# Kernel optimization log

Hardware: AMD Instinct MI355X
Metric: run time of the kernel (lower is better)

Reference implementation:

```python
import math
import jax, jax.numpy as jnp
import numpy as np

B, T, C, H, E, K = 2, 2048, 1024, 16, 8, 2
HID = 4 * C
D = C // H

def new_gelu(x):
    return 0.5 * x * (1.0 + jnp.tanh(math.sqrt(2.0 / math.pi) * (x + 0.044715 * x ** 3)))

def layer_norm(x, g, b, eps=1e-5):
    mu = jnp.mean(x, axis=-1, keepdims=True)
    var = jnp.var(x, axis=-1, keepdims=True)
    return (x - mu) / jnp.sqrt(var + eps) * g + b

def setup_inputs():
    key = jax.random.key(0)
    ks = jax.random.split(key, 8)
    s = 0.02
    return {
        'x': jax.random.normal(ks[0], (B, T, C), jnp.float32),
        'ln1_g': jnp.ones((C,), jnp.float32), 'ln1_b': jnp.zeros((C,), jnp.float32),
        'ln2_g': jnp.ones((C,), jnp.float32), 'ln2_b': jnp.zeros((C,), jnp.float32),
        'attn_w': (jax.random.normal(ks[1], (C, 3 * C), jnp.float32) * s),
        'attn_b': jnp.zeros((3 * C,), jnp.float32),
        'proj_w': (jax.random.normal(ks[2], (C, C), jnp.float32) * s),
        'proj_b': jnp.zeros((C,), jnp.float32),
        'router_w': (jax.random.normal(ks[3], (C, E), jnp.float32) * s),
        'fc_w': (jax.random.normal(ks[4], (E, C, HID), jnp.float32) * s),
        'fc_b': jnp.zeros((E, HID), jnp.float32),
        'pj_w': (jax.random.normal(ks[5], (E, HID, C), jnp.float32) * s),
        'pj_b': jnp.zeros((E, C), jnp.float32),
    }

def reference(x, ln1_g, ln1_b, ln2_g, ln2_b, attn_w, attn_b, proj_w, proj_b, router_w, fc_w, fc_b, pj_w, pj_b):
    # --- causal self-attention with residual ---
    h = layer_norm(x, ln1_g, ln1_b)
    qkv = h @ attn_w + attn_b                              # [B,T,3C]
    q, k, v = jnp.split(qkv, 3, axis=-1)
    q = q.reshape(B, T, H, D).transpose(0, 2, 1, 3)        # [B,H,T,D]
    k = k.reshape(B, T, H, D).transpose(0, 2, 1, 3)
    v = v.reshape(B, T, H, D).transpose(0, 2, 1, 3)
    att = jnp.einsum('bhqd,bhkd->bhqk', q, k) * (1.0 / math.sqrt(D))
    mask = jnp.tril(jnp.ones((T, T), dtype=bool))
    att = jnp.where(mask, att, jnp.float32(-jnp.inf))
    att = jax.nn.softmax(att, axis=-1)                     # dropout p=0 (eval)
    y = jnp.einsum('bhqk,bhkd->bhqd', att, v)
    y = y.transpose(0, 2, 1, 3).reshape(B, T, C)
    x = x + (y @ proj_w + proj_b)
    # --- MoE FFN with residual ---
    h2 = layer_norm(x, ln2_g, ln2_b).reshape(B * T, C)     # [N,C]
    logits = h2 @ router_w                                 # [N,E]
    probs = jax.nn.softmax(logits, axis=-1)
    topk_p, topk_i = jax.lax.top_k(probs, K)               # [N,K]
    topk_p = topk_p / jnp.sum(topk_p, axis=-1, keepdims=True)
    # dense combine weights: zero outside selected experts (same math as scatter)
    gate = jnp.zeros((B * T, E), h2.dtype).at[jnp.arange(B * T)[:, None], topk_i].add(topk_p)
    out = jnp.zeros_like(h2)
    for e in range(E):  # fixed small expert loop
        he = new_gelu(h2 @ fc_w[e] + fc_b[e])              # [N,HID]
        out = out + gate[:, e:e + 1] * (he @ pj_w[e] + pj_b[e])
    return x + out.reshape(B, T, C)
```

## Files before the change

### kernel.cpp

```cpp
#include <hip/hip_runtime.h>
#include <math.h>


typedef __bf16 b16v8 __attribute__((ext_vector_type(8)));
typedef float f32x4 __attribute__((ext_vector_type(4)));

#define MFMA(a, b, c) __builtin_amdgcn_mfma_f32_16x16x32_bf16(a, b, c, 0, 0, 0)

#define GLOAD_LDS16(g, l)                                          \
  __builtin_amdgcn_global_load_lds(                                \
      (const __attribute__((address_space(1))) void*)(g),          \
      (__attribute__((address_space(3))) void*)(l), 16, 0, 0)

constexpr int Bc = 2, Tc = 2048, Cc = 1024, Hc = 16, Dc = 64;
constexpr int Nc = Bc * Tc;
constexpr int HIDc = 4096;
constexpr int Ec = 8;
constexpr int NPAIR = Nc * 2;
constexpr int NRBMAX = NPAIR / 128 + Ec;
constexpr float LOG2E = 1.4426950408889634f;

__device__ inline unsigned short f32_bf16(float f) {
  union { float f; unsigned u; } x; x.f = f;
  unsigned r = x.u + 0x7fffu + ((x.u >> 16) & 1u);
  return (unsigned short)(r >> 16);
}

__device__ inline float gelu_f(float x) {
  float t = 2.3021188f * x * (1.f + 0.044715f * x * x);
  float e = __builtin_amdgcn_exp2f(-t);
  return x * __builtin_amdgcn_rcpf(1.f + e);
}

__device__ inline int swz32(int row, int g) {
  return row * 32 + ((g ^ ((row >> 1) & 3)) * 8);
}

__global__ __launch_bounds__(256) void convT_kernel(
    const float* __restrict__ src, unsigned short* __restrict__ dst,
    int K, int N) {
  const size_t sb = (size_t)blockIdx.z * K * N;
  const int n0 = blockIdx.x * 32, k0 = blockIdx.y * 32;
  __shared__ float t[32][33];
  const int tx = threadIdx.x & 31, ty = threadIdx.x >> 5;
#pragma unroll
  for (int j = 0; j < 4; ++j)
    t[ty + j * 8][tx] = src[sb + (size_t)(k0 + ty + j * 8) * N + n0 + tx];
  __syncthreads();
#pragma unroll
  for (int j = 0; j < 4; ++j)
    dst[sb + (size_t)(n0 + ty + j * 8) * K + k0 + tx] = f32_bf16(t[tx][ty + j * 8]);
}

__global__ __launch_bounds__(256) void ln1_kernel(
    const float* __restrict__ x, const float* __restrict__ g,
    const float* __restrict__ b, unsigned short* __restrict__ out) {
  const int row = blockIdx.x;
  const int tid = threadIdx.x;
  const float* xr = x + (size_t)row * Cc;
  float v[4]; float s = 0.f, q = 0.f;
#pragma unroll
  for (int j = 0; j < 4; ++j) { v[j] = xr[tid + j * 256]; s += v[j]; q += v[j] * v[j]; }
#pragma unroll
  for (int m = 1; m <= 32; m <<= 1) { s += __shfl_xor(s, m); q += __shfl_xor(q, m); }
  __shared__ float red[2][4];
  const int w = tid >> 6;
  if ((tid & 63) == 0) { red[0][w] = s; red[1][w] = q; }
  __syncthreads();
  s = red[0][0] + red[0][1] + red[0][2] + red[0][3];
  q = red[1][0] + red[1][1] + red[1][2] + red[1][3];
  const float mean = s * (1.f / Cc);
  const float var = q * (1.f / Cc) - mean * mean;
  const float rstd = rsqrtf(var + 1e-5f);
#pragma unroll
  for (int j = 0; j < 4; ++j) {
    int c = tid + j * 256;
    out[(size_t)row * Cc + c] = f32_bf16((v[j] - mean) * rstd * g[c] + b[c]);
  }
}

__global__ __launch_bounds__(256) void ln2_router_kernel(
    const float* __restrict__ x, const float* __restrict__ g,
    const float* __restrict__ b, const float* __restrict__ rw,
    unsigned short* __restrict__ out, int* __restrict__ tki, float* __restrict__ tkp) {
  const int row = blockIdx.x;
  const int tid = threadIdx.x;
  const float* xr = x + (size_t)row * Cc;
  float v[4]; float s = 0.f, q = 0.f;
#pragma unroll
  for (int j = 0; j < 4; ++j) { v[j] = xr[tid + j * 256]; s += v[j]; q += v[j] * v[j]; }
#pragma unroll
  for (int m = 1; m <= 32; m <<= 1) { s += __shfl_xor(s, m); q += __shfl_xor(q, m); }
  __shared__ float red[2][4];
  const int w = tid >> 6;
  if ((tid & 63) == 0) { red[0][w] = s; red[1][w] = q; }
  __syncthreads();
  s = red[0][0] + red[0][1] + red[0][2] + red[0][3];
  q = red[1][0] + red[1][1] + red[1][2] + red[1][3];
  const float mean = s * (1.f / Cc);
  const float var = q * (1.f / Cc) - mean * mean;
  const float rstd = rsqrtf(var + 1e-5f);
  float lg[8] = {0.f, 0.f, 0.f, 0.f, 0.f, 0.f, 0.f, 0.f};
#pragma unroll
  for (int j = 0; j < 4; ++j) {
    int c = tid + j * 256;
    float nv = (v[j] - mean) * rstd * g[c] + b[c];
    out[(size_t)row * Cc + c] = f32_bf16(nv);
    const float* rwc = rw + c * 8;
#pragma unroll
    for (int e = 0; e < 8; ++e) lg[e] += nv * rwc[e];
  }
#pragma unroll
  for (int m = 1; m <= 32; m <<= 1) {
#pragma unroll
    for (int e = 0; e < 8; ++e) lg[e] += __shfl_xor(lg[e], m);
  }
  __shared__ float rl[4][8];
  if ((tid & 63) == 0) {
#pragma unroll
    for (int e = 0; e < 8; ++e) rl[w][e] = lg[e];
  }
  __syncthreads();
  if (tid == 0) {
    float L[8];
#pragma unroll
    for (int e = 0; e < 8; ++e) L[e] = rl[0][e] + rl[1][e] + rl[2][e] + rl[3][e];
    int i1 = 0;
    for (int e = 1; e < 8; ++e) if (L[e] > L[i1]) i1 = e;
    int i2 = (i1 == 0) ? 1 : 0;
    for (int e = 0; e < 8; ++e) if (e != i1 && L[e] > L[i2]) i2 = e;
    float e2 = expf(L[i2] - L[i1]);
    float inv = 1.f / (1.f + e2);
    tki[row * 2] = i1; tki[row * 2 + 1] = i2;
    tkp[row * 2] = inv; tkp[row * 2 + 1] = e2 * inv;
  }
}

__global__ __launch_bounds__(256) void count_kernel(
    const int* __restrict__ tki, int* __restrict__ counts) {
  int n = blockIdx.x * 256 + threadIdx.x;
  if (n >= Nc) return;
  atomicAdd(&counts[tki[n * 2]], 1);
  atomicAdd(&counts[tki[n * 2 + 1]], 1);
}

__global__ void scan_kernel(const int* __restrict__ counts,
                            int* __restrict__ eoff, int* __restrict__ cursor,
                            int* __restrict__ tbl_e, int* __restrict__ tbl_r0,
                            int* __restrict__ tbl_n) {
  if (threadIdx.x == 0 && blockIdx.x == 0) {
    int s = 0, nb = 0;
    for (int e = 0; e < Ec; ++e) {
      eoff[e] = s; cursor[e] = s;
      for (int r = 0; r < counts[e]; r += 128) {
        tbl_e[nb] = e; tbl_r0[nb] = r; ++nb;
      }
      s += counts[e];
    }
    eoff[Ec] = s;
    *tbl_n = nb;
  }
}

__global__ __launch_bounds__(256) void assign_kernel(
    const int* __restrict__ tki, int* __restrict__ cursor,
    int* __restrict__ slot_tok, int* __restrict__ tok2slot) {
  int n = blockIdx.x * 256 + threadIdx.x;
  if (n >= Nc) return;
#pragma unroll
  for (int kk = 0; kk < 2; ++kk) {
    int e = tki[n * 2 + kk];
    int slot = atomicAdd(&cursor[e], 1);
    slot_tok[slot] = n;
    tok2slot[n * 2 + kk] = slot;
  }
}

struct GArgs {
  const unsigned short* A;
  const unsigned short* Bt;
  const float* bias;
  int M, N, K, lda, ldb, klen;
  size_t Bstride; int biasStride;
  const int* eoff;
  const int* slot_tok;
  const int* tbl_e;
  const int* tbl_r0;
  const int* tbl_n;
  float* outF;
  const float* resid;
  unsigned short* outB;
  unsigned short* outK;
  unsigned short* outV;
};

template <int MODE>
__global__ __launch_bounds__(256) void gemm128b(GArgs g) {
  int e = 0, s0 = 0, Meff = g.M, row0;
  if constexpr (MODE == 2 || MODE == 3) {
    if ((int)blockIdx.y >= *g.tbl_n) return;
    e = g.tbl_e[blockIdx.y];
    row0 = g.tbl_r0[blockIdx.y];
    s0 = g.eoff[e];
    Meff = g.eoff[e + 1] - s0;
  } else {
    row0 = blockIdx.y * 128;
  }
  const int kh = (MODE == 3) ? blockIdx.z : 0;
  const int col0 = blockIdx.x * 128;
  const int kbase = kh * g.klen;

  __shared__ __align__(16) unsigned short As[128 * 32];
  __shared__ __align__(16) unsigned short Bs[128 * 32];

  const int tid = threadIdx.x;
  const int lane = tid & 63, w = tid >> 6;
  const int wr = w >> 1, wc = w & 1;
  const int fr = lane & 15, fg = lane >> 4;

  const unsigned short* Bt = g.Bt + (size_t)e * g.Bstride;
  const float* bias = g.bias + (size_t)e * g.biasStride;

  size_t aaddr[2], baddr[2];
#pragma unroll
  for (int i = 0; i < 2; ++i) {
    int pos = i * 256 + tid;
    int r = pos >> 2;
    int c8 = ((pos & 3) ^ ((r >> 1) & 3)) * 8;
    int gr = row0 + r;
    if (gr >= Meff) gr = Meff - 1;
    int srcrow;
    if constexpr (MODE == 2) srcrow = g.slot_tok[s0 + gr];
    else if constexpr (MODE == 3) srcrow = s0 + gr;
    else srcrow = gr;
    aaddr[i] = (size_t)srcrow * g.lda + kbase + c8;
    baddr[i] = (size_t)(col0 + r) * g.ldb + kbase + c8;
  }

  auto STAGE = [&](int k0) {
#pragma unroll
    for (int i = 0; i < 2; ++i) {
      GLOAD_LDS16(g.A + aaddr[i] + k0, &As[i * 2048 + w * 512]);
      GLOAD_LDS16(Bt + baddr[i] + k0, &Bs[i * 2048 + w * 512]);
    }
  };

  f32x4 acc[4][4] = {};
  const int nt = g.klen / 32;

  for (int t = 0; t < nt; ++t) {
    if (t) __syncthreads();
    STAGE(t * 32);
    __syncthreads();
    b16v8 af[4], bf_[4];
#pragma unroll
    for (int mi = 0; mi < 4; ++mi)
      af[mi] = *(const b16v8*)&As[swz32(wr * 64 + mi * 16 + fr, fg)];
#pragma unroll
    for (int ni = 0; ni < 4; ++ni)
      bf_[ni] = *(const b16v8*)&Bs[swz32(wc * 64 + ni * 16 + fr, fg)];
#pragma unroll
    for (int mi = 0; mi < 4; ++mi)
#pragma unroll
      for (int ni = 0; ni < 4; ++ni)
        acc[mi][ni] = MFMA(af[mi], bf_[ni], acc[mi][ni]);
  }

  float* outF3 = nullptr;
  if constexpr (MODE == 3) outF3 = g.outF + (size_t)kh * NPAIR * Cc;

#pragma unroll
  for (int mi = 0; mi < 4; ++mi) {
#pragma unroll
    for (int ni = 0; ni < 4; ++ni) {
#pragma unroll
      for (int rr = 0; rr < 4; ++rr) {
        int row = row0 + wr * 64 + mi * 16 + fg * 4 + rr;
        int col = col0 + wc * 64 + ni * 16 + fr;
        if (row >= Meff) continue;
        float bval = bias[col];
        if constexpr (MODE == 3) { if (kh != 0) bval = 0.f; }
        float val = acc[mi][ni][rr] + bval;
        if constexpr (MODE == 0) {
          int bb = row >> 11, tt = row & (Tc - 1);
          int which = col >> 10, cj = col & (Cc - 1);
          int hd = cj >> 6, d = cj & 63;
          if (which == 0)
            g.outB[(((size_t)(bb * Hc + hd)) * Tc + tt) * Dc + d] = f32_bf16(val);
          else if (which == 1)
            g.outK[(((size_t)(bb * Hc + hd)) * Tc + tt) * Dc + d] = f32_bf16(val);
          else
            g.outV[(((size_t)(bb * Hc + hd)) * Dc + d) * Tc + tt] = f32_bf16(val);
        } else if constexpr (MODE == 1) {
          size_t o = (size_t)row * g.N + col;
          g.outF[o] = val + g.resid[o];
        } else if constexpr (MODE == 2) {
          g.outB[(size_t)(s0 + row) * g.N + col] = f32_bf16(gelu_f(val));
        } else {
          outF3[(size_t)(s0 + row) * g.N + col] = val;
        }
      }
    }
  }
}

__global__ __launch_bounds__(512) void attn_kernel(
    const unsigned short* __restrict__ q, const unsigned short* __restrict__ k,
    const unsigned short* __restrict__ v, unsigned short* __restrict__ y) {
  const int qt = blockIdx.x, bh = blockIdx.y;
  const int qbase = qt * 128;
  __shared__ __align__(16) unsigned short ldsK[64][72];
  __shared__ __align__(16) unsigned short ldsVT[64][72];
  __shared__ __align__(16) unsigned short ldsP[8][16][72];
  const int tid = threadIdx.x, lane = tid & 63, w = tid >> 6;
  const int fr = lane & 15, fg = lane >> 4;
  const size_t base = (size_t)bh * Tc * Dc;
  const int qrow = qbase + w * 16 + fr;
  b16v8 qa0 = *(const b16v8*)(q + base + (size_t)qrow * Dc + fg * 8);
  b16v8 qa1 = *(const b16v8*)(q + base + (size_t)qrow * Dc + 32 + fg * 8);
  float m[4], lsum[4] = {0.f, 0.f, 0.f, 0.f};
#pragma unroll
  for (int r = 0; r < 4; ++r) m[r] = -3.0e38f;
  f32x4 oacc[4] = {};
  constexpr float SC = 0.125f * LOG2E;

  const int sr = tid >> 3, scb = (tid & 7) * 8;
  const int ntile = (qbase + 128) / 64;

  *(uint4*)&ldsK[sr][scb]  = *(const uint4*)(k + base + (size_t)sr * Dc + scb);
  *(uint4*)&ldsVT[sr][scb] = *(const uint4*)(v + base + (size_t)sr * Tc + scb);
  __syncthreads();

  for (int ti = 0; ti < ntile; ++ti) {
    const int kb = ti * 64;
    uint4 kreg, vreg;
    const bool more = (ti + 1 < ntile);
    if (more) {
      const int kn = kb + 64;
      kreg = *(const uint4*)(k + base + (size_t)(kn + sr) * Dc + scb);
      vreg = *(const uint4*)(v + base + (size_t)sr * Tc + kn + scb);
    }

    f32x4 s[4];
#pragma unroll
    for (int ni = 0; ni < 4; ++ni) {
      b16v8 kb0 = *(const b16v8*)&ldsK[ni * 16 + fr][fg * 8];
      b16v8 kb1 = *(const b16v8*)&ldsK[ni * 16 + fr][32 + fg * 8];
      f32x4 z = {};
      z = MFMA(qa0, kb0, z);
      z = MFMA(qa1, kb1, z);
      s[ni] = z;
    }
    const bool diag = (kb + 64 > qbase + w * 16);
#pragma unroll
    for (int ni = 0; ni < 4; ++ni) {
#pragma unroll
      for (int r = 0; r < 4; ++r) {
        float sv = s[ni][r] * SC;
        if (diag) {
          int gq = qbase + w * 16 + fg * 4 + r;
          int kv = kb + ni * 16 + fr;
          if (kv > gq) sv = -3.0e38f;
        }
        s[ni][r] = sv;
      }
    }
#pragma unroll
    for (int r = 0; r < 4; ++r) {
      float mx = fmaxf(fmaxf(s[0][r], s[1][r]), fmaxf(s[2][r], s[3][r]));
#pragma unroll
      for (int msk = 1; msk <= 8; msk <<= 1) mx = fmaxf(mx, __shfl_xor(mx, msk));
      float mnew = fmaxf(m[r], mx);
      float alpha = __builtin_amdgcn_exp2f(m[r] - mnew);
      float psum = 0.f;
#pragma unroll
      for (int ni = 0; ni < 4; ++ni) {
        float pp = __builtin_amdgcn_exp2f(s[ni][r] - mnew);
        s[ni][r] = pp;
        psum += pp;
      }
#pragma unroll
      for (int msk = 1; msk <= 8; msk <<= 1) psum += __shfl_xor(psum, msk);
      lsum[r] = lsum[r] * alpha + psum;
      m[r] = mnew;
#pragma unroll
      for (int ni = 0; ni < 4; ++ni) {
        oacc[ni][r] = oacc[ni][r] * alpha;
        ldsP[w][fg * 4 + r][ni * 16 + fr] = f32_bf16(s[ni][r]);
      }
    }
    asm volatile("s_waitcnt lgkmcnt(0)" ::: "memory");
    __builtin_amdgcn_sched_barrier(0);
    b16v8 pa0 = *(const b16v8*)&ldsP[w][fr][fg * 8];
    b16v8 pa1 = *(const b16v8*)&ldsP[w][fr][32 + fg * 8];
#pragma unroll
    for (int ni = 0; ni < 4; ++ni) {
      b16v8 vb0 = *(const b16v8*)&ldsVT[ni * 16 + fr][fg * 8];
      b16v8 vb1 = *(const b16v8*)&ldsVT[ni * 16 + fr][32 + fg * 8];
      oacc[ni] = MFMA(pa0, vb0, oacc[ni]);
      oacc[ni] = MFMA(pa1, vb1, oacc[ni]);
    }

    if (more) {
      __syncthreads();
      *(uint4*)&ldsK[sr][scb]  = kreg;
      *(uint4*)&ldsVT[sr][scb] = vreg;
      __syncthreads();
    }
  }

  const int bb = bh >> 4, hh = bh & 15;
#pragma unroll
  for (int r = 0; r < 4; ++r) {
    float rl = __builtin_amdgcn_rcpf(lsum[r]);
#pragma unroll
    for (int ni = 0; ni < 4; ++ni) {
      int t = qbase + w * 16 + fg * 4 + r;
      int d = ni * 16 + fr;
      y[((size_t)(bb * Tc + t)) * Cc + hh * Dc + d] = f32_bf16(oacc[ni][r] * rl);
    }
  }
}

__global__ __launch_bounds__(256) void combine_kernel(
    const float* __restrict__ pair, const float* __restrict__ tkp,
    const int* __restrict__ tok2slot, float* __restrict__ out) {
  const int n = blockIdx.x;
  const int c4 = threadIdx.x * 4;
  const int s0 = tok2slot[n * 2], s1 = tok2slot[n * 2 + 1];
  const float p0 = tkp[n * 2], p1 = tkp[n * 2 + 1];
  const float* pb = pair + (size_t)NPAIR * Cc;
  float4 a0 = *(const float4*)&pair[(size_t)s0 * Cc + c4];
  float4 a1 = *(const float4*)&pb[(size_t)s0 * Cc + c4];
  float4 b0 = *(const float4*)&pair[(size_t)s1 * Cc + c4];
  float4 b1 = *(const float4*)&pb[(size_t)s1 * Cc + c4];
  float4 o = *(float4*)&out[(size_t)n * Cc + c4];
  o.x += p0 * (a0.x + a1.x) + p1 * (b0.x + b1.x);
  o.y += p0 * (a0.y + a1.y) + p1 * (b0.y + b1.y);
  o.z += p0 * (a0.z + a1.z) + p1 * (b0.z + b1.z);
  o.w += p0 * (a0.w + a1.w) + p1 * (b0.w + b1.w);
  *(float4*)&out[(size_t)n * Cc + c4] = o;
}

extern "C" void kernel_launch(void* const* d_in, const int* in_sizes, int n_in,
                              void* d_out, int out_size, void* d_ws, size_t ws_size,
                              hipStream_t stream) {
  const float* x        = (const float*)d_in[0];
  const float* ln1_g    = (const float*)d_in[1];
  const float* ln1_b    = (const float*)d_in[2];
  const float* ln2_g    = (const float*)d_in[3];
  const float* ln2_b    = (const float*)d_in[4];
  const float* attn_w   = (const float*)d_in[5];
  const float* attn_b   = (const float*)d_in[6];
  const float* proj_w   = (const float*)d_in[7];
  const float* proj_b   = (const float*)d_in[8];
  const float* router_w = (const float*)d_in[9];
  const float* fc_w     = (const float*)d_in[10];
  const float* fc_b     = (const float*)d_in[11];
  const float* pj_w     = (const float*)d_in[12];
  const float* pj_b     = (const float*)d_in[13];
  float* out = (float*)d_out;

  char* ws = (char*)d_ws;
  size_t off = 0;
  auto alloc = [&](size_t bytes) -> void* {
    void* p = ws + off;
    off = (off + bytes + 255) & ~(size_t)255;
    return p;
  };
  unsigned short* attn_wT = (unsigned short*)alloc((size_t)3 * Cc * Cc * 2);
  unsigned short* proj_wT = (unsigned short*)alloc((size_t)Cc * Cc * 2);
  unsigned short* fc_wT   = (unsigned short*)alloc((size_t)Ec * HIDc * Cc * 2);
  unsigned short* pj_wT   = (unsigned short*)alloc((size_t)Ec * Cc * HIDc * 2);
  unsigned short* h    = (unsigned short*)alloc((size_t)Nc * Cc * 2);
  unsigned short* qb   = (unsigned short*)alloc((size_t)Nc * Cc * 2);
  unsigned short* kbuf = (unsigned short*)alloc((size_t)Nc * Cc * 2);
  unsigned short* vbuf = (unsigned short*)alloc((size_t)Nc * Cc * 2);
  unsigned short* ybuf = (unsigned short*)alloc((size_t)Nc * Cc * 2);
  unsigned short* he   = (unsigned short*)alloc((size_t)NPAIR * HIDc * 2);
  float* pairout = (float*)alloc((size_t)2 * NPAIR * Cc * 4);
  int*   tki     = (int*)alloc((size_t)Nc * 2 * 4);
  float* tkp     = (float*)alloc((size_t)Nc * 2 * 4);
  int*   counts  = (int*)alloc(Ec * 4);
  int*   eoff    = (int*)alloc((Ec + 1) * 4);
  int*   cursor  = (int*)alloc(Ec * 4);
  int*   slot_tok= (int*)alloc((size_t)NPAIR * 4);
  int*   tok2slot= (int*)alloc((size_t)Nc * 2 * 4);
  int*   tbl_e   = (int*)alloc(NRBMAX * 4);
  int*   tbl_r0  = (int*)alloc(NRBMAX * 4);
  int*   tbl_n   = (int*)alloc(4);
  (void)ws_size; (void)in_sizes; (void)n_in; (void)out_size;

  convT_kernel<<<dim3(3 * Cc / 32, Cc / 32, 1), 256, 0, stream>>>(attn_w, attn_wT, Cc, 3 * Cc);
  convT_kernel<<<dim3(Cc / 32, Cc / 32, 1), 256, 0, stream>>>(proj_w, proj_wT, Cc, Cc);
  convT_kernel<<<dim3(HIDc / 32, Cc / 32, Ec), 256, 0, stream>>>(fc_w, fc_wT, Cc, HIDc);
  convT_kernel<<<dim3(Cc / 32, HIDc / 32, Ec), 256, 0, stream>>>(pj_w, pj_wT, HIDc, Cc);

  ln1_kernel<<<Nc, 256, 0, stream>>>(x, ln1_g, ln1_b, h);

  {
    GArgs a = {};
    a.A = h; a.Bt = attn_wT; a.bias = attn_b;
    a.M = Nc; a.N = 3 * Cc; a.K = Cc; a.lda = Cc; a.ldb = Cc; a.klen = Cc;
    a.outB = qb; a.outK = kbuf; a.outV = vbuf;
    gemm128b<0><<<dim3(3 * Cc / 128, Nc / 128, 1), 256, 0, stream>>>(a);
  }

  attn_kernel<<<dim3(Tc / 128, Bc * Hc), 512, 0, stream>>>(qb, kbuf, vbuf, ybuf);

  {
    GArgs p = {};
    p.A = ybuf; p.Bt = proj_wT; p.bias = proj_b;
    p.M = Nc; p.N = Cc; p.K = Cc; p.lda = Cc; p.ldb = Cc; p.klen = Cc;
    p.outF = out; p.resid = x;
    gemm128b<1><<<dim3(Cc / 128, Nc / 128, 1), 256, 0, stream>>>(p);
  }

  ln2_router_kernel<<<Nc, 256, 0, stream>>>(out, ln2_g, ln2_b, router_w, h, tki, tkp);

  hipMemsetAsync(counts, 0, Ec * sizeof(int), stream);
  count_kernel<<<(Nc + 255) / 256, 256, 0, stream>>>(tki, counts);
  scan_kernel<<<1, 64, 0, stream>>>(counts, eoff, cursor, tbl_e, tbl_r0, tbl_n);
  assign_kernel<<<(Nc + 255) / 256, 256, 0, stream>>>(tki, cursor, slot_tok, tok2slot);

  {
    GArgs f = {};
    f.A = h; f.Bt = fc_wT; f.bias = fc_b;
    f.M = Nc; f.N = HIDc; f.K = Cc; f.lda = Cc; f.ldb = Cc; f.klen = Cc;
    f.Bstride = (size_t)HIDc * Cc; f.biasStride = HIDc;
    f.eoff = eoff; f.slot_tok = slot_tok;
    f.tbl_e = tbl_e; f.tbl_r0 = tbl_r0; f.tbl_n = tbl_n;
    f.outB = he;
    gemm128b<2><<<dim3(HIDc / 128, NRBMAX, 1), 256, 0, stream>>>(f);
  }

  {
    GArgs pj = {};
    pj.A = he; pj.Bt = pj_wT; pj.bias = pj_b;
    pj.M = Nc; pj.N = Cc; pj.K = HIDc; pj.lda = HIDc; pj.ldb = HIDc; pj.klen = HIDc / 2;
    pj.Bstride = (size_t)Cc * HIDc; pj.biasStride = Cc;
    pj.eoff = eoff;
    pj.tbl_e = tbl_e; pj.tbl_r0 = tbl_r0; pj.tbl_n = tbl_n;
    pj.outF = pairout;
    gemm128b<3><<<dim3(Cc / 128, NRBMAX, 2), 256, 0, stream>>>(pj);
  }

  combine_kernel<<<Nc, 256, 0, stream>>>(pairout, tkp, tok2slot, out);
}
```

Before: 669.3 us.

## Replace expert block table with 1D grid interleaving experts across workgroups

Removes the serial block-table construction in the scan kernel and the table indirection in the MoE GEMMs. Each workgroup now decodes its expert from the low 3 bits of a 1D block id, then its row block and column/K-half from the remaining bits. Adjacent workgroups therefore land on different experts, which changes scheduling order and cache reuse of expert weights. The grid is sized for up to 32 row blocks per expert, so many workgroups launch only to exit early, and any expert with more than 4096 routed tokens would have rows that are never processed.

```diff
diff --git a/kernel.cpp b/kernel.cpp
--- a/kernel.cpp
+++ b/kernel.cpp
@@ -17,7 +17,6 @@
 constexpr int HIDc = 4096;
 constexpr int Ec = 8;
 constexpr int NPAIR = Nc * 2;
-constexpr int NRBMAX = NPAIR / 128 + Ec;
 constexpr float LOG2E = 1.4426950408889634f;
 
 __device__ inline unsigned short f32_bf16(float f) {
@@ -145,20 +144,11 @@
 }
 
 __global__ void scan_kernel(const int* __restrict__ counts,
-                            int* __restrict__ eoff, int* __restrict__ cursor,
-                            int* __restrict__ tbl_e, int* __restrict__ tbl_r0,
-                            int* __restrict__ tbl_n) {
+                            int* __restrict__ eoff, int* __restrict__ cursor) {
   if (threadIdx.x == 0 && blockIdx.x == 0) {
-    int s = 0, nb = 0;
-    for (int e = 0; e < Ec; ++e) {
-      eoff[e] = s; cursor[e] = s;
-      for (int r = 0; r < counts[e]; r += 128) {
-        tbl_e[nb] = e; tbl_r0[nb] = r; ++nb;
-      }
-      s += counts[e];
-    }
+    int s = 0;
+    for (int e = 0; e < Ec; ++e) { eoff[e] = s; cursor[e] = s; s += counts[e]; }
     eoff[Ec] = s;
-    *tbl_n = nb;
   }
 }
 
@@ -184,9 +174,6 @@
   size_t Bstride; int biasStride;
   const int* eoff;
   const int* slot_tok;
-  const int* tbl_e;
-  const int* tbl_r0;
-  const int* tbl_n;
   float* outF;
   const float* resid;
   unsigned short* outB;
@@ -196,18 +183,24 @@
 
 template <int MODE>
 __global__ __launch_bounds__(256) void gemm128b(GArgs g) {
-  int e = 0, s0 = 0, Meff = g.M, row0;
+  int e = 0, s0 = 0, Meff = g.M, row0, col0, kh = 0;
   if constexpr (MODE == 2 || MODE == 3) {
-    if ((int)blockIdx.y >= *g.tbl_n) return;
-    e = g.tbl_e[blockIdx.y];
-    row0 = g.tbl_r0[blockIdx.y];
+    const int id = blockIdx.x;
+    e = id & 7;
+    const int local = id >> 3;
     s0 = g.eoff[e];
     Meff = g.eoff[e + 1] - s0;
+    const int nrb = (Meff + 127) >> 7;
+    const int rb = local & 31;
+    if (rb >= nrb) return;
+    int ck = local >> 5;
+    if constexpr (MODE == 3) { kh = ck & 1; ck >>= 1; }
+    row0 = rb * 128;
+    col0 = ck * 128;
   } else {
     row0 = blockIdx.y * 128;
-  }
-  const int kh = (MODE == 3) ? blockIdx.z : 0;
-  const int col0 = blockIdx.x * 128;
+    col0 = blockIdx.x * 128;
+  }
   const int kbase = kh * g.klen;
 
   __shared__ __align__(16) unsigned short As[128 * 32];
@@ -486,9 +479,6 @@
   int*   cursor  = (int*)alloc(Ec * 4);
   int*   slot_tok= (int*)alloc((size_t)NPAIR * 4);
   int*   tok2slot= (int*)alloc((size_t)Nc * 2 * 4);
-  int*   tbl_e   = (int*)alloc(NRBMAX * 4);
-  int*   tbl_r0  = (int*)alloc(NRBMAX * 4);
-  int*   tbl_n   = (int*)alloc(4);
   (void)ws_size; (void)in_sizes; (void)n_in; (void)out_size;
 
   convT_kernel<<<dim3(3 * Cc / 32, Cc / 32, 1), 256, 0, stream>>>(attn_w, attn_wT, Cc, 3 * Cc);
@@ -520,7 +510,7 @@
 
   hipMemsetAsync(counts, 0, Ec * sizeof(int), stream);
   count_kernel<<<(Nc + 255) / 256, 256, 0, stream>>>(tki, counts);
-  scan_kernel<<<1, 64, 0, stream>>>(counts, eoff, cursor, tbl_e, tbl_r0, tbl_n);
+  scan_kernel<<<1, 64, 0, stream>>>(counts, eoff, cursor);
   assign_kernel<<<(Nc + 255) / 256, 256, 0, stream>>>(tki, cursor, slot_tok, tok2slot);
 
   {
@@ -529,9 +519,8 @@
     f.M = Nc; f.N = HIDc; f.K = Cc; f.lda = Cc; f.ldb = Cc; f.klen = Cc;
     f.Bstride = (size_t)HIDc * Cc; f.biasStride = HIDc;
     f.eoff = eoff; f.slot_tok = slot_tok;
-    f.tbl_e = tbl_e; f.tbl_r0 = tbl_r0; f.tbl_n = tbl_n;
     f.outB = he;
-    gemm128b<2><<<dim3(HIDc / 128, NRBMAX, 1), 256, 0, stream>>>(f);
+    gemm128b<2><<<8 * 32 * 32, 256, 0, stream>>>(f);
   }
 
   {
@@ -540,9 +529,8 @@
     pj.M = Nc; pj.N = Cc; pj.K = HIDc; pj.lda = HIDc; pj.ldb = HIDc; pj.klen = HIDc / 2;
     pj.Bstride = (size_t)Cc * HIDc; pj.biasStride = Cc;
     pj.eoff = eoff;
-    pj.tbl_e = tbl_e; pj.tbl_r0 = tbl_r0; pj.tbl_n = tbl_n;
     pj.outF = pairout;
-    gemm128b<3><<<dim3(Cc / 128, NRBMAX, 2), 256, 0, stream>>>(pj);
+    gemm128b<3><<<8 * 16 * 32, 256, 0, stream>>>(pj);
   }
 
   combine_kernel<<<Nc, 256, 0, stream>>>(pairout, tkp, tok2slot, out);
```

New measurement: 688.9 us. +2.9%, slower.
